# Performance work log

Hardware: AMD Instinct MI355X
Metric: run time of the kernel (lower is better)

## Reference

```python
import jax, jax.numpy as jnp
import numpy as np

# module hyperparameters (init_kwargs)
WEIGHT = 2e-9
SIGMA_RGB = 0.15   # images in [0,1]; equals canonical 15/255
SIGMA_XY = 100.0
SCALE = 0.5

N, C, K, H, W = 4, 3, 21, 128, 128


def _nearest(x, oh, ow):
    """torch F.interpolate(mode='nearest'): src = floor(dst * in/out)."""
    h, w = x.shape[-2], x.shape[-1]
    iy = jnp.floor(jnp.arange(oh) * (h / oh)).astype(jnp.int32)
    ix = jnp.floor(jnp.arange(ow) * (w / ow)).astype(jnp.int32)
    return x[..., iy[:, None], ix[None, :]]


def _bilinear(x, oh, ow):
    """torch F.interpolate(mode='bilinear', align_corners=False)."""
    h, w = x.shape[-2], x.shape[-1]

    def coords(o, s):
        c = (jnp.arange(o, dtype=jnp.float32) + 0.5) * (s / o) - 0.5
        c = jnp.clip(c, 0.0, s - 1.0)
        c0 = jnp.floor(c).astype(jnp.int32)
        c1 = jnp.minimum(c0 + 1, s - 1)
        return c0, c1, c - c0

    y0, y1, wy = coords(oh, h)
    x0, x1, wx = coords(ow, w)
    wy = wy[:, None]
    wx = wx[None, :]
    v00 = x[..., y0[:, None], x0[None, :]]
    v01 = x[..., y0[:, None], x1[None, :]]
    v10 = x[..., y1[:, None], x0[None, :]]
    v11 = x[..., y1[:, None], x1[None, :]]
    top = v00 * (1.0 - wx) + v01 * wx
    bot = v10 * (1.0 - wx) + v11 * wx
    return top * (1.0 - wy) + bot * wy


def setup_inputs() -> dict:
    key = jax.random.key(0)
    k1, k2 = jax.random.split(key)
    images = jax.random.uniform(k1, (N, C, H, W), jnp.float32)
    segmentations = jax.random.uniform(k2, (N, K, H, W), jnp.float32)
    ROIs = jnp.ones((N, H, W), jnp.float32)
    return {"images": images, "segmentations": segmentations, "ROIs": ROIs}


def reference(images, segmentations, ROIs):
    oh, ow = int(H * SCALE), int(W * SCALE)
    img_s = _nearest(images, oh, ow)           # [N,3,oh,ow]
    seg_s = _bilinear(segmentations, oh, ow)   # [N,K,oh,ow]
    roi_s = _nearest(ROIs, oh, ow)             # [N,oh,ow]
    seg_m = seg_s * roi_s[:, None]             # seg * ROI (per class)
    sxy = SIGMA_XY * SCALE

    # exact dense Gaussian bilateral kernel that the permutohedral lattice
    # (bilateralfilter_batch) approximates: k(i,j) = exp(-|p_i-p_j|^2/(2 sxy^2)
    #                                                  -|I_i-I_j|^2/(2 srgb^2))
    yy, xx = jnp.meshgrid(jnp.arange(oh, dtype=jnp.float32),
                          jnp.arange(ow, dtype=jnp.float32), indexing="ij")
    pos = jnp.stack([xx, yy], 0) / sxy         # [2,oh,ow]

    def per_image(img, seg):
        feat = jnp.concatenate([pos, img / SIGMA_RGB], 0).reshape(5, -1).T  # [P,5]
        sq = jnp.sum(feat * feat, axis=-1)                                  # [P]
        d2 = jnp.maximum(sq[:, None] + sq[None, :] - 2.0 * (feat @ feat.T), 0.0)
        Wk = jnp.exp(-0.5 * d2)                                             # [P,P]
        s = seg.reshape(K, -1)                                              # [K,P]
        AS = s @ Wk                                                         # filtered seg
        return jnp.sum(s * AS)

    vals = jax.vmap(per_image)(img_s, seg_m)   # [N]
    loss = -(jnp.sum(vals)) / N                # densecrf_loss
    return WEIGHT * loss
```

## Files before the change

kernel.cpp:

```cpp
#include <hip/hip_runtime.h>

#define NIMG 4
#define CCH  3
#define KCH  21
#define HIN  128
#define WIN  128
#define OH   64
#define OW   64
#define PPX  (OH*OW)
#define NPIX (NIMG*PPX)

#define PRE2 1.20112241f

#define SEGW  24
#define FEATW 8

#define BLOCK  256
#define JCHUNK 256
#define IBLK   64

#define NSLOT  64

typedef _Float16 half_t;
typedef half_t half8  __attribute__((ext_vector_type(8)));
typedef float  f32x4v __attribute__((ext_vector_type(4)));

#define FEATH_OFF ((size_t)NPIX*SEGW*2)
#define SQF_OFF   (FEATH_OFF + (size_t)NPIX*FEATW*2)
#define SLOT_OFF  (SQF_OFF + (size_t)NPIX*4)

__global__ __launch_bounds__(BLOCK) void crf_prep(const float* __restrict__ img,
                                                  const float* __restrict__ seg,
                                                  const float* __restrict__ roi,
                                                  half_t* __restrict__ segH,
                                                  half_t* __restrict__ featH,
                                                  float* __restrict__ sqF,
                                                  float* __restrict__ slots) {
    int g  = blockIdx.x * BLOCK + threadIdx.x;
    int q  = g >> 14;
    int pl = g & (NPIX - 1);
    int n  = pl >> 12;
    int p  = pl & (PPX - 1);
    int y = p >> 6, x = p & 63;
    int y2 = 2 * y, x2 = 2 * x;

    if (q < SEGW) {
        float v = 0.0f;
        if (q < KCH) {
            const float* s0 = seg + (((size_t)n * KCH + q) * HIN + y2) * WIN + x2;
            float r = roi[((size_t)n * HIN + y2) * WIN + x2];
            v = 0.25f * (s0[0] + s0[1] + s0[WIN] + s0[WIN + 1]) * r;
        }
        segH[(size_t)pl * SEGW + q] = (half_t)v;
    } else if (q == 24) {
        float fx = (float)x * (PRE2 / 50.0f);
        float fy = (float)y * (PRE2 / 50.0f);
        const size_t ib = (((size_t)n * CCH) * HIN + y2) * WIN + x2;
        float fr = img[ib]                         * (PRE2 / 0.15f);
        float fg = img[ib + (size_t)HIN * WIN]     * (PRE2 / 0.15f);
        float fb = img[ib + 2 * (size_t)HIN * WIN] * (PRE2 / 0.15f);
        half_t h0 = (half_t)fx, h1 = (half_t)fy, h2 = (half_t)fr,
               h3 = (half_t)fg, h4 = (half_t)fb;
        half8 fh = {h0, h1, h2, h3, h4, (half_t)0, (half_t)0, (half_t)0};
        *(half8*)(featH + (size_t)pl * FEATW) = fh;
        float a0 = (float)h0, a1 = (float)h1, a2 = (float)h2,
              a3 = (float)h3, a4 = (float)h4;
        sqF[pl] = 0.5f * (a0 * a0 + a1 * a1 + a2 * a2 + a3 * a3 + a4 * a4);
    } else if (q == 25) {
        if (pl < NSLOT) slots[pl * 16] = 0.0f;
    }
}

__global__ __launch_bounds__(BLOCK, 8) void crf_main(const half_t* __restrict__ segH,
                                                     const half_t* __restrict__ featH,
                                                     const float* __restrict__ sqF,
                                                     float* __restrict__ slots) {
    const int bx = blockIdx.x;
    const int n  = blockIdx.y;

    int g = 0;
#pragma unroll
    for (int t = 1; t < 16; ++t) {
        int off = 64 * t - 2 * t * (t - 1);
        if (bx >= off) g = t;
    }
    int rem = bx - (64 * g - 2 * g * (g - 1));
    int c   = 16 - g;
    int iq  = (rem >= c) + (rem >= 2 * c) + (rem >= 3 * c);
    int I   = 4 * g + iq;
    int J   = g + (rem - iq * c);
    const bool diag = (J == (I >> 2));

    const half_t* segN  = segH  + (size_t)n * PPX * SEGW;
    const half_t* featN = featH + (size_t)n * PPX * FEATW;
    const float*  sqN   = sqF   + (size_t)n * PPX;

    __shared__ alignas(16) half_t segJ[JCHUNK * SEGW];
    __shared__ alignas(16) half_t featJ[JCHUNK * FEATW];
    __shared__ alignas(16) half_t zrow[8];
    __shared__ float hJ[JCHUNK];
    __shared__ float wsum[BLOCK / 64];

    const int tid  = threadIdx.x;
    const int lane = tid & 63, wv = tid >> 6;
    const int m = lane & 15, quad = lane >> 4;
    const int i0 = I * IBLK + wv * 16;
    const int j0 = J * JCHUNK;
    const int kq = (quad < 2) ? quad : 2;

    half8 hz = {};

    half8 aseg  = *(const half8*)(segN  + (size_t)(i0 + m) * SEGW + kq * 8);
    half8 afeat = *(const half8*)(featN + (size_t)(i0 + m) * FEATW);
    f32x4v hi   = *(const f32x4v*)(sqN + i0 + quad * 4);
    if (quad == 3) aseg  = hz;
    if (quad != 0) afeat = hz;
    f32x4v nh = -hi;

    {
        const f32x4v* gsrc = (const f32x4v*)(segN + (size_t)j0 * SEGW);
        f32x4v* ldst = (f32x4v*)segJ;
#pragma unroll
        for (int v = 0; v < 3; ++v) ldst[tid + v * BLOCK] = gsrc[tid + v * BLOCK];
        ((f32x4v*)featJ)[tid] = ((const f32x4v*)(featN + (size_t)j0 * FEATW))[tid];
        hJ[tid] = sqN[j0 + tid];
        if (tid < 8) zrow[tid] = (half_t)0;
    }
    __syncthreads();

    const half_t* bsp; int bstep;
    if (quad == 3) { bsp = zrow;                       bstep = 0; }
    else           { bsp = segJ + m * SEGW + quad * 8; bstep = 16 * SEGW; }
    const half_t* bfp; int fstep;
    if (quad == 0) { bfp = featJ + m * FEATW;          fstep = 16 * FEATW; }
    else           { bfp = zrow;                       fstep = 0; }

    float racc = 0.0f;
    const f32x4v zero4 = {0.0f, 0.0f, 0.0f, 0.0f};

#pragma unroll 4
    for (int jt = 0; jt < JCHUNK / 16; ++jt) {
        half8 bseg = *(const half8*)bsp;  bsp += bstep;
        half8 bft  = *(const half8*)bfp;  bfp += fstep;
        float hc = hJ[jt * 16 + m];

        f32x4v c4 = {nh[0] - hc, nh[1] - hc, nh[2] - hc, nh[3] - hc};
        f32x4v E  = __builtin_amdgcn_mfma_f32_16x16x32_f16(afeat, bft, c4, 0, 0, 0);
        f32x4v Gs = __builtin_amdgcn_mfma_f32_16x16x32_f16(aseg, bseg, zero4, 0, 0, 0);

        if (!diag) {
#pragma unroll
            for (int r = 0; r < 4; ++r)
                racc = fmaf(__builtin_amdgcn_exp2f(E[r]), Gs[r], racc);
        } else {
            const int jg = j0 + jt * 16 + m;
#pragma unroll
            for (int r = 0; r < 4; ++r) {
                int ig = i0 + quad * 4 + r;
                float sel = (jg > ig) ? 1.0f : ((jg == ig) ? 0.0f : -100000.0f);
                racc = fmaf(__builtin_amdgcn_exp2f(E[r] + sel), Gs[r], racc);
            }
        }
    }

#pragma unroll
    for (int off = 32; off > 0; off >>= 1) racc += __shfl_down(racc, off);
    if (lane == 0) wsum[wv] = racc;
    __syncthreads();
    if (tid == 0) {
        float s = wsum[0] + wsum[1] + wsum[2] + wsum[3];
        if (!diag) s *= 2.0f;
        int slot = (bx + 544 * n) & (NSLOT - 1);
        atomicAdd(&slots[slot * 16], s);
    }
}

__global__ __launch_bounds__(64) void crf_final(const float* __restrict__ slots,
                                                float* __restrict__ out) {
    int lane = threadIdx.x;
    float v = slots[lane * 16];
#pragma unroll
    for (int off = 32; off > 0; off >>= 1) v += __shfl_down(v, off);
    if (lane == 0) out[0] = v * (-5.0e-10f);
}

extern "C" void kernel_launch(void* const* d_in, const int* in_sizes, int n_in,
                              void* d_out, int out_size, void* d_ws, size_t ws_size,
                              hipStream_t stream) {
    const float* img = (const float*)d_in[0];
    const float* seg = (const float*)d_in[1];
    const float* roi = (const float*)d_in[2];
    float* out = (float*)d_out;

    char* wsb = (char*)d_ws;
    half_t* segH  = (half_t*)(wsb);
    half_t* featH = (half_t*)(wsb + FEATH_OFF);
    float*  sqF   = (float*)(wsb + SQF_OFF);
    float*  slots = (float*)(wsb + SLOT_OFF);

    crf_prep<<<(NPIX * 32) / BLOCK, BLOCK, 0, stream>>>(img, seg, roi,
                                                        segH, featH, sqF, slots);

    dim3 grid(544, NIMG);
    crf_main<<<grid, BLOCK, 0, stream>>>(segH, featH, sqF, slots);

    crf_final<<<1, 64, 0, stream>>>(slots, out);
}
```

Measured before the change: 75.18 us.

## Double i-tile per block, skip masked diagonal tiles, fuse final reduction via ticket

```diff
diff --git a/kernel.cpp b/kernel.cpp
--- a/kernel.cpp
+++ b/kernel.cpp
@@ -17,7 +17,10 @@
 
 #define BLOCK  256
 #define JCHUNK 256
-#define IBLK   64
+#define IBLK   128
+
+#define NBLK_IMG 272
+#define NBLK_TOT (NBLK_IMG*NIMG)
 
 #define NSLOT  64
 
@@ -68,28 +71,25 @@
         sqF[pl] = 0.5f * (a0 * a0 + a1 * a1 + a2 * a2 + a3 * a3 + a4 * a4);
     } else if (q == 25) {
         if (pl < NSLOT) slots[pl * 16] = 0.0f;
+        if (pl == NSLOT) ((unsigned*)slots)[NSLOT * 16] = 0u;
     }
 }
 
-__global__ __launch_bounds__(BLOCK, 8) void crf_main(const half_t* __restrict__ segH,
+__global__ __launch_bounds__(BLOCK, 6) void crf_main(const half_t* __restrict__ segH,
                                                      const half_t* __restrict__ featH,
                                                      const float* __restrict__ sqF,
-                                                     float* __restrict__ slots) {
+                                                     float* __restrict__ slots,
+                                                     float* __restrict__ out) {
     const int bx = blockIdx.x;
     const int n  = blockIdx.y;
 
-    int g = 0;
+    int J = 0;
 #pragma unroll
     for (int t = 1; t < 16; ++t) {
-        int off = 64 * t - 2 * t * (t - 1);
-        if (bx >= off) g = t;
-    }
-    int rem = bx - (64 * g - 2 * g * (g - 1));
-    int c   = 16 - g;
-    int iq  = (rem >= c) + (rem >= 2 * c) + (rem >= 3 * c);
-    int I   = 4 * g + iq;
-    int J   = g + (rem - iq * c);
-    const bool diag = (J == (I >> 2));
+        if (bx >= t * t + t) J = t;
+    }
+    const int I = bx - (J * J + J);
+    const bool diag = ((I >> 1) == J);
 
     const half_t* segN  = segH  + (size_t)n * PPX * SEGW;
     const half_t* featN = featH + (size_t)n * PPX * FEATW;
@@ -100,22 +100,27 @@
     __shared__ alignas(16) half_t zrow[8];
     __shared__ float hJ[JCHUNK];
     __shared__ float wsum[BLOCK / 64];
+    __shared__ int lastBlk;
 
     const int tid  = threadIdx.x;
     const int lane = tid & 63, wv = tid >> 6;
     const int m = lane & 15, quad = lane >> 4;
-    const int i0 = I * IBLK + wv * 16;
-    const int j0 = J * JCHUNK;
-    const int kq = (quad < 2) ? quad : 2;
+    const int i0a = I * IBLK + wv * 16;
+    const int i0b = i0a + 64;
+    const int j0  = J * JCHUNK;
+    const int kq  = (quad < 2) ? quad : 2;
 
     half8 hz = {};
 
-    half8 aseg  = *(const half8*)(segN  + (size_t)(i0 + m) * SEGW + kq * 8);
-    half8 afeat = *(const half8*)(featN + (size_t)(i0 + m) * FEATW);
-    f32x4v hi   = *(const f32x4v*)(sqN + i0 + quad * 4);
-    if (quad == 3) aseg  = hz;
-    if (quad != 0) afeat = hz;
-    f32x4v nh = -hi;
+    half8 aseg0  = *(const half8*)(segN  + (size_t)(i0a + m) * SEGW + kq * 8);
+    half8 aseg1  = *(const half8*)(segN  + (size_t)(i0b + m) * SEGW + kq * 8);
+    half8 afeat0 = *(const half8*)(featN + (size_t)(i0a + m) * FEATW);
+    half8 afeat1 = *(const half8*)(featN + (size_t)(i0b + m) * FEATW);
+    f32x4v hi0   = *(const f32x4v*)(sqN + i0a + quad * 4);
+    f32x4v hi1   = *(const f32x4v*)(sqN + i0b + quad * 4);
+    if (quad == 3) { aseg0 = hz; aseg1 = hz; }
+    if (quad != 0) { afeat0 = hz; afeat1 = hz; }
+    f32x4v nh0 = -hi0, nh1 = -hi1;
 
     {
         const f32x4v* gsrc = (const f32x4v*)(segN + (size_t)j0 * SEGW);
@@ -138,50 +143,63 @@
     float racc = 0.0f;
     const f32x4v zero4 = {0.0f, 0.0f, 0.0f, 0.0f};
 
-#pragma unroll 4
+#define DO_SET(AFEAT, ASEG, NH, I0S)                                              \
+    {                                                                             \
+        f32x4v c4 = {(NH)[0] - hc, (NH)[1] - hc, (NH)[2] - hc, (NH)[3] - hc};     \
+        f32x4v E  = __builtin_amdgcn_mfma_f32_16x16x32_f16(AFEAT, bft, c4, 0, 0, 0);   \
+        f32x4v Gs = __builtin_amdgcn_mfma_f32_16x16x32_f16(ASEG, bseg, zero4, 0, 0, 0);\
+        if (!diag) {                                                              \
+            _Pragma("unroll")                                                     \
+            for (int r = 0; r < 4; ++r)                                           \
+                racc = fmaf(__builtin_amdgcn_exp2f(E[r]), Gs[r], racc);           \
+        } else {                                                                  \
+            _Pragma("unroll")                                                     \
+            for (int r = 0; r < 4; ++r) {                                         \
+                int ig = (I0S) + quad * 4 + r;                                    \
+                float sel = (jg > ig) ? 1.0f : ((jg == ig) ? 0.0f : -100000.0f);  \
+                racc = fmaf(__builtin_amdgcn_exp2f(E[r] + sel), Gs[r], racc);     \
+            }                                                                     \
+        }                                                                         \
+    }
+
+#pragma unroll 2
     for (int jt = 0; jt < JCHUNK / 16; ++jt) {
         half8 bseg = *(const half8*)bsp;  bsp += bstep;
         half8 bft  = *(const half8*)bfp;  bfp += fstep;
         float hc = hJ[jt * 16 + m];
-
-        f32x4v c4 = {nh[0] - hc, nh[1] - hc, nh[2] - hc, nh[3] - hc};
-        f32x4v E  = __builtin_amdgcn_mfma_f32_16x16x32_f16(afeat, bft, c4, 0, 0, 0);
-        f32x4v Gs = __builtin_amdgcn_mfma_f32_16x16x32_f16(aseg, bseg, zero4, 0, 0, 0);
-
-        if (!diag) {
-#pragma unroll
-            for (int r = 0; r < 4; ++r)
-                racc = fmaf(__builtin_amdgcn_exp2f(E[r]), Gs[r], racc);
-        } else {
-            const int jg = j0 + jt * 16 + m;
-#pragma unroll
-            for (int r = 0; r < 4; ++r) {
-                int ig = i0 + quad * 4 + r;
-                float sel = (jg > ig) ? 1.0f : ((jg == ig) ? 0.0f : -100000.0f);
-                racc = fmaf(__builtin_amdgcn_exp2f(E[r] + sel), Gs[r], racc);
-            }
-        }
-    }
+        const int jg   = j0 + jt * 16 + m;
+        const int jmax = j0 + jt * 16 + 15;
+
+        if (!diag || jmax >= i0a) DO_SET(afeat0, aseg0, nh0, i0a);
+        if (!diag || jmax >= i0b) DO_SET(afeat1, aseg1, nh1, i0b);
+    }
+#undef DO_SET
 
 #pragma unroll
     for (int off = 32; off > 0; off >>= 1) racc += __shfl_down(racc, off);
     if (lane == 0) wsum[wv] = racc;
     __syncthreads();
+
+    unsigned* ticket = (unsigned*)&slots[NSLOT * 16];
     if (tid == 0) {
         float s = wsum[0] + wsum[1] + wsum[2] + wsum[3];
         if (!diag) s *= 2.0f;
-        int slot = (bx + 544 * n) & (NSLOT - 1);
+        int slot = (bx + NBLK_IMG * n) & (NSLOT - 1);
         atomicAdd(&slots[slot * 16], s);
-    }
-}
-
-__global__ __launch_bounds__(64) void crf_final(const float* __restrict__ slots,
-                                                float* __restrict__ out) {
-    int lane = threadIdx.x;
-    float v = slots[lane * 16];
-#pragma unroll
-    for (int off = 32; off > 0; off >>= 1) v += __shfl_down(v, off);
-    if (lane == 0) out[0] = v * (-5.0e-10f);
+        __threadfence();
+        unsigned t = __hip_atomic_fetch_add(ticket, 1u, __ATOMIC_ACQ_REL,
+                                            __HIP_MEMORY_SCOPE_AGENT);
+        lastBlk = (t == NBLK_TOT - 1);
+    }
+    __syncthreads();
+
+    if (lastBlk && tid < 64) {
+        float v = __hip_atomic_load(&slots[tid * 16], __ATOMIC_ACQUIRE,
+                                    __HIP_MEMORY_SCOPE_AGENT);
+#pragma unroll
+        for (int off = 32; off > 0; off >>= 1) v += __shfl_down(v, off);
+        if (tid == 0) out[0] = v * (-5.0e-10f);
+    }
 }
 
 extern "C" void kernel_launch(void* const* d_in, const int* in_sizes, int n_in,
@@ -198,11 +216,9 @@
     float*  sqF   = (float*)(wsb + SQF_OFF);
     float*  slots = (float*)(wsb + SLOT_OFF);
 
-    crf_prep<<<(NPIX * 32) / BLOCK, BLOCK, 0, stream>>>(img, seg, roi,
+    crf_prep<<<(NPIX * 26) / BLOCK, BLOCK, 0, stream>>>(img, seg, roi,
                                                         segH, featH, sqF, slots);
 
-    dim3 grid(544, NIMG);
-    crf_main<<<grid, BLOCK, 0, stream>>>(segH, featH, sqF, slots);
-
-    crf_final<<<1, 64, 0, stream>>>(slots, out);
+    dim3 grid(NBLK_IMG, NIMG);
+    crf_main<<<grid, BLOCK, 0, stream>>>(segH, featH, sqF, slots, out);
 }
```

After: 101.0 us. 34.3% more time.
